# Kernel tuning notes

Measured on AMD Instinct MI355X. Metric: run time of the kernel, lower is better.

Reference implementation:

```python
import jax, jax.numpy as jnp
import numpy as np

QLEN, MLEN, BSZ = 1024, 1024, 2
D_MODEL, H, D_HEAD, D_FF = 1024, 16, 64, 4096
KLEN = QLEN + MLEN


def _ln(x, g, b, eps=1e-5):
    mu = jnp.mean(x, axis=-1, keepdims=True)
    var = jnp.var(x, axis=-1, keepdims=True)
    return (x - mu) * jax.lax.rsqrt(var + eps) * g + b


def _rel_shift(x):
    # x: [q, k, b, n] -> Transformer-XL relative shift
    q, k, b, n = x.shape
    zp = jnp.zeros((q, 1, b, n), x.dtype)
    xp = jnp.concatenate([zp, x], axis=1).reshape(k + 1, q, b, n)[1:]
    return xp.reshape(q, k, b, n)


def setup_inputs() -> dict:
    key = jax.random.key(0)
    ks = jax.random.split(key, 12)
    s = 0.02
    inp = {
        "input_": jax.random.normal(ks[0], (QLEN, BSZ, D_MODEL), jnp.float32),
        "mems": jax.random.normal(ks[1], (MLEN, BSZ, D_MODEL), jnp.float32),
        "pos_emb": jax.random.normal(ks[2], (KLEN, 1, D_MODEL), jnp.float32),
        # True = masked. Causal with memory: query i sees keys j <= i + MLEN
        "mask_tgt": jnp.triu(jnp.ones((QLEN, KLEN), bool), k=MLEN + 1),
        "ln1_g": jnp.ones((D_MODEL,), jnp.float32),
        "ln1_b": jnp.zeros((D_MODEL,), jnp.float32),
        "qkv_w": jax.random.normal(ks[3], (D_MODEL, 3 * H * D_HEAD), jnp.float32) * s,
        "qkv_b": jnp.zeros((3 * H * D_HEAD,), jnp.float32),
        "r_w": jax.random.normal(ks[4], (D_MODEL, H * D_HEAD), jnp.float32) * s,
        "r_w_bias": jax.random.normal(ks[5], (H, D_HEAD), jnp.float32) * s,
        "r_r_bias": jax.random.normal(ks[6], (H, D_HEAD), jnp.float32) * s,
        "o_w": jax.random.normal(ks[7], (H * D_HEAD, D_MODEL), jnp.float32) * s,
        "ln2_g": jnp.ones((D_MODEL,), jnp.float32),
        "ln2_b": jnp.zeros((D_MODEL,), jnp.float32),
        "ff_w1": jax.random.normal(ks[8], (D_MODEL, D_FF), jnp.float32) * s,
        "ff_b1": jnp.zeros((D_FF,), jnp.float32),
        "ff_w2": jax.random.normal(ks[9], (D_FF, D_MODEL), jnp.float32) * s,
        "ff_b2": jnp.zeros((D_MODEL,), jnp.float32),
    }
    return inp


def reference(input_, mems, pos_emb, mask_tgt, ln1_g, ln1_b, qkv_w, qkv_b,
              r_w, r_w_bias, r_r_bias, o_w, ln2_g, ln2_b,
              ff_w1, ff_b1, ff_w2, ff_b2):
    qlen, bsz, _ = input_.shape
    # --- pre-norm (applied to both current input and mems) ---
    q_in = _ln(input_, ln1_g, ln1_b)
    m_in = _ln(mems, ln1_g, ln1_b)
    cat = jnp.concatenate([m_in, q_in], axis=0)            # [klen, b, d]
    klen = cat.shape[0]
    heads = cat @ qkv_w + qkv_b                            # [klen, b, 3*h*dh]
    w_q, w_k, w_v = jnp.split(heads, 3, axis=-1)
    w_q = w_q[-qlen:].reshape(qlen, bsz, H, D_HEAD)        # [q, b, h, dh]
    w_k = w_k.reshape(klen, bsz, H, D_HEAD)
    w_v = w_v.reshape(klen, bsz, H, D_HEAD)
    r_k = (pos_emb[:, 0] @ r_w).reshape(klen, H, D_HEAD)   # [k, h, dh]

    AC = jnp.einsum('ibnd,jbnd->ijbn', w_q + r_w_bias, w_k)
    BD = jnp.einsum('ibnd,jnd->ijbn', w_q + r_r_bias, r_k)
    BD = _rel_shift(BD)
    scale = 1.0 / np.sqrt(D_HEAD)
    score = (AC + BD) * scale                              # [q, k, b, h]
    score = jnp.where(mask_tgt[:, :, None, None], -1e30, score)
    prob = jax.nn.softmax(score, axis=1)
    attn = jnp.einsum('ijbn,jbnd->ibnd', prob, w_v).reshape(qlen, bsz, H * D_HEAD)
    attn_out = attn @ o_w                                  # [q, b, d]
    x = input_ + attn_out                                  # residual (dropout = eval)

    # --- FFN block ---
    y = _ln(x, ln2_g, ln2_b)
    y = jax.nn.relu(y @ ff_w1 + ff_b1) @ ff_w2 + ff_b2
    return x + y
```

## Files before the change

### kernel.cpp

```cpp
#include <hip/hip_runtime.h>


typedef unsigned short u16;
typedef unsigned int   u32;
typedef __attribute__((ext_vector_type(8))) short bf16x8;
typedef __attribute__((ext_vector_type(4))) float f32x4;

struct alignas(16) U128 { u32 x[4]; };
struct alignas(16) F128 { float f[4]; };
struct alignas(8)  U64  { u32 x[2]; };

#define DEV static __device__ __forceinline__
#define MF(a, b, c) __builtin_amdgcn_mfma_f32_16x16x32_bf16((a), (b), (c), 0, 0, 0)

typedef __attribute__((address_space(1))) u32 as1_u32;
typedef __attribute__((address_space(3))) u32 as3_u32;
DEV void gload16(const void* g, void* l) {
  __builtin_amdgcn_global_load_lds((as1_u32*)g, (as3_u32*)l, 16, 0, 0);
}

DEV u16 f2bf(float f) {
  union { float f; u32 u; } v; v.f = f;
  u32 r = v.u + 0x7fffu + ((v.u >> 16) & 1u);
  return (u16)(r >> 16);
}
DEV float bf2f(u16 h) {
  union { u32 u; float f; } v; v.u = ((u32)h) << 16;
  return v.f;
}

__global__ __launch_bounds__(256) void ln_fuse(
    const u16* __restrict__ p0, const u16* __restrict__ p1,
    const u16* __restrict__ p2, const u16* __restrict__ p3,
    const float* __restrict__ resid, const float* __restrict__ g,
    const float* __restrict__ b, float* __restrict__ X, u16* __restrict__ YN)
{
  int row = blockIdx.x, tid = threadIdx.x;
  U64 a = ((const U64*)(p0 + (size_t)row * 1024))[tid];
  U64 c = ((const U64*)(p1 + (size_t)row * 1024))[tid];
  U64 d = ((const U64*)(p2 + (size_t)row * 1024))[tid];
  U64 e = ((const U64*)(p3 + (size_t)row * 1024))[tid];
  F128 rv = ((const F128*)(resid + (size_t)row * 1024))[tid];
  float x[4];
#pragma unroll
  for (int k = 0; k < 2; k++) {
    x[2*k]   = bf2f((u16)a.x[k]) + bf2f((u16)c.x[k]) + bf2f((u16)d.x[k]) + bf2f((u16)e.x[k]) + rv.f[2*k];
    x[2*k+1] = bf2f((u16)(a.x[k] >> 16)) + bf2f((u16)(c.x[k] >> 16)) + bf2f((u16)(d.x[k] >> 16)) + bf2f((u16)(e.x[k] >> 16)) + rv.f[2*k+1];
  }
  F128 xo;
#pragma unroll
  for (int j = 0; j < 4; j++) xo.f[j] = x[j];
  *(F128*)(X + (size_t)row * 1024 + tid * 4) = xo;

  float s = x[0] + x[1] + x[2] + x[3];
  float q = x[0]*x[0] + x[1]*x[1] + x[2]*x[2] + x[3]*x[3];
#pragma unroll
  for (int off = 1; off < 64; off <<= 1) {
    s += __shfl_xor(s, off); q += __shfl_xor(q, off);
  }
  __shared__ float sh[8];
  int wid = tid >> 6;
  if ((tid & 63) == 0) { sh[wid] = s; sh[4 + wid] = q; }
  __syncthreads();
  s = sh[0] + sh[1] + sh[2] + sh[3];
  q = sh[4] + sh[5] + sh[6] + sh[7];
  float mu = s * (1.0f / 1024.0f);
  float rs = rsqrtf(q * (1.0f / 1024.0f) - mu * mu + 1e-5f);
  F128 g4 = ((const F128*)g)[tid];
  F128 b4 = ((const F128*)b)[tid];
  union { u16 h[4]; U64 u; } o;
#pragma unroll
  for (int j = 0; j < 4; j++)
    o.h[j] = f2bf((x[j] - mu) * rs * g4.f[j] + b4.f[j]);
  *(U64*)(YN + (size_t)row * 1024 + tid * 4) = o.u;
}

__global__ __launch_bounds__(256) void prep_weights(
    const float* __restrict__ qkvw, const float* __restrict__ rw,
    const float* __restrict__ oww, const float* __restrict__ fw1,
    const float* __restrict__ fw2, const float* __restrict__ pos,
    const float* __restrict__ mems, const float* __restrict__ input_,
    const float* __restrict__ ln1g, const float* __restrict__ ln1b,
    u16* __restrict__ WT_QKV, u16* __restrict__ WT_R, u16* __restrict__ WT_O,
    u16* __restrict__ WT_F1, u16* __restrict__ WT_F2, u16* __restrict__ POSB,
    u16* __restrict__ CATLN)
{
  int id = blockIdx.x, tid = threadIdx.x;
  if (id >= 5376) {
    int row = id - 5376;
    const float* s_ = (row < 2048) ? mems + (size_t)row * 1024
                                   : input_ + (size_t)(row - 2048) * 1024;
    F128 v = ((const F128*)s_)[tid];
    float s = v.f[0] + v.f[1] + v.f[2] + v.f[3];
    float q = v.f[0]*v.f[0] + v.f[1]*v.f[1] + v.f[2]*v.f[2] + v.f[3]*v.f[3];
#pragma unroll
    for (int off = 1; off < 64; off <<= 1) {
      s += __shfl_xor(s, off); q += __shfl_xor(q, off);
    }
    __shared__ float sh[8];
    int wid = tid >> 6;
    if ((tid & 63) == 0) { sh[wid] = s; sh[4 + wid] = q; }
    __syncthreads();
    s = sh[0] + sh[1] + sh[2] + sh[3];
    q = sh[4] + sh[5] + sh[6] + sh[7];
    float mu = s * (1.0f / 1024.0f);
    float rs = rsqrtf(q * (1.0f / 1024.0f) - mu * mu + 1e-5f);
    F128 g4 = ((const F128*)ln1g)[tid];
    F128 b4 = ((const F128*)ln1b)[tid];
    union { u16 h[4]; U64 u; } o;
#pragma unroll
    for (int j = 0; j < 4; j++)
      o.h[j] = f2bf((v.f[j] - mu) * rs * g4.f[j] + b4.f[j]);
    *(U64*)(CATLN + (size_t)row * 1024 + tid * 4) = o.u;
    return;
  }
  if (id >= 3328) {
    int i = (id - 3328) * 256 + tid;
    F128 v = ((const F128*)pos)[i];
    union { u16 h[4]; U64 u; } o;
#pragma unroll
    for (int j = 0; j < 4; j++) o.h[j] = f2bf(v.f[j]);
    ((U64*)POSB)[i] = o.u;
    return;
  }
  const float* W; u16* Wt; int K, N, rem;
  if (id < 768)       { W = qkvw; Wt = WT_QKV; K = 1024; N = 3072; rem = id; }
  else if (id < 1024) { W = rw;   Wt = WT_R;   K = 1024; N = 1024; rem = id - 768; }
  else if (id < 1280) { W = oww;  Wt = WT_O;   K = 1024; N = 1024; rem = id - 1024; }
  else if (id < 2304) { W = fw1;  Wt = WT_F1;  K = 1024; N = 4096; rem = id - 1280; }
  else                { W = fw2;  Wt = WT_F2;  K = 4096; N = 1024; rem = id - 2304; }
  int nn = N >> 6;
  int k0 = (rem / nn) * 64, n0 = (rem % nn) * 64;
  __shared__ float t[64][65];
  int r = tid >> 6, c = tid & 63;
#pragma unroll
  for (int i = 0; i < 16; i++)
    t[r + i * 4][c] = W[(size_t)(k0 + r + i * 4) * N + n0 + c];
  __syncthreads();
#pragma unroll
  for (int i = 0; i < 16; i++) {
    int n = r + i * 4;
    Wt[(size_t)(n0 + n) * K + k0 + c] = f2bf(t[c][n]);
  }
}

template <int EPI, int NSPLIT>
__global__ __launch_bounds__(256, 2) void gemm_bt(
    const u16* __restrict__ A, const u16* __restrict__ Bt,
    u16* __restrict__ outb, const float* __restrict__ bias,
    u16* __restrict__ p0, u16* __restrict__ p1,
    u16* __restrict__ p2, u16* __restrict__ p3,
    int M, int N, int K)
{
  __shared__ u16 As[2][128 * 64];
  __shared__ u16 Bs[2][128 * 64];
  int tid = threadIdx.x;
  int m0 = blockIdx.x * 128, n0 = blockIdx.y * 128;
  int lane = tid & 63, wid = tid >> 6;
  int wr = wid >> 1, wc = wid & 1;
  f32x4 acc[4][4] = {};

  const int Kc = K / NSPLIT;
  const int kbase = (NSPLIT > 1) ? (int)blockIdx.z * Kc : 0;

  const int lrow = wid * 8 + (lane >> 3);
  const int lcol = 8 * ((lane & 7) ^ (lane >> 3));
  const u16* Ag = A  + (size_t)(m0 + lrow) * K + kbase + lcol;
  const u16* Bg = Bt + (size_t)(n0 + lrow) * K + kbase + lcol;

  auto stage = [&](int buf, int k0) {
#pragma unroll
    for (int i = 0; i < 4; i++) {
      gload16(Ag + (size_t)i * 32 * K + k0, &As[buf][(i * 4 + wid) * 512]);
      gload16(Bg + (size_t)i * 32 * K + k0, &Bs[buf][(i * 4 + wid) * 512]);
    }
  };

  const int rswz = 8 * (lane & 7);
  stage(0, 0);
  __syncthreads();
  int cur = 0;
  for (int k0 = 0; k0 < Kc; k0 += 64) {
    if (k0 + 64 < Kc) stage(cur ^ 1, k0 + 64);
    bf16x8 af[2][4], bfr[2][4];
#pragma unroll
    for (int kc = 0; kc < 2; kc++) {
      int cb = (kc * 32 + (lane >> 4) * 8) ^ rswz;
#pragma unroll
      for (int f = 0; f < 4; f++) {
        af[kc][f]  = *(const bf16x8*)&As[cur][(wr * 64 + f * 16 + (lane & 15)) * 64 + cb];
        bfr[kc][f] = *(const bf16x8*)&Bs[cur][(wc * 64 + f * 16 + (lane & 15)) * 64 + cb];
      }
    }
    __builtin_amdgcn_s_setprio(1);
#pragma unroll
    for (int kc = 0; kc < 2; kc++)
#pragma unroll
      for (int fi = 0; fi < 4; fi++)
#pragma unroll
        for (int fj = 0; fj < 4; fj++)
          acc[fi][fj] = MF(af[kc][fi], bfr[kc][fj], acc[fi][fj]);
    __builtin_amdgcn_s_setprio(0);
    __syncthreads();
    cur ^= 1;
  }

  u16* part = nullptr;
  if constexpr (NSPLIT > 1) {
    part = (blockIdx.z == 0) ? p0 : (blockIdx.z == 1) ? p1
         : (blockIdx.z == 2) ? p2 : p3;
  }
#pragma unroll
  for (int fi = 0; fi < 4; fi++)
#pragma unroll
    for (int fj = 0; fj < 4; fj++) {
      int col = n0 + wc * 64 + fj * 16 + (lane & 15);
      float bvv = (NSPLIT == 1 && bias != nullptr) ? bias[col] : 0.0f;
#pragma unroll
      for (int r = 0; r < 4; r++) {
        int row = m0 + wr * 64 + fi * 16 + (lane >> 4) * 4 + r;
        float v = acc[fi][fj][r] + bvv;
        if constexpr (NSPLIT > 1) {
          part[(size_t)row * N + col] = f2bf(v);
        } else {
          if constexpr (EPI == 1) v = fmaxf(v, 0.0f);
          outb[(size_t)row * N + col] = f2bf(v);
        }
      }
    }
}

template <int NS, int EPI>
__global__ __launch_bounds__(256) void reduce_splitb(
    const u16* __restrict__ p0, const u16* __restrict__ p1,
    const u16* __restrict__ p2, const u16* __restrict__ p3,
    const float* __restrict__ bias, const float* __restrict__ resid,
    u16* __restrict__ outb, float* __restrict__ outf, int N)
{
  int e = (blockIdx.x * 256 + threadIdx.x) * 8;
  U128 a = *(const U128*)(p0 + e);
  U128 c = *(const U128*)(p1 + e);
  float v[8];
#pragma unroll
  for (int k = 0; k < 4; k++) {
    v[2*k]   = bf2f((u16)a.x[k]) + bf2f((u16)c.x[k]);
    v[2*k+1] = bf2f((u16)(a.x[k] >> 16)) + bf2f((u16)(c.x[k] >> 16));
  }
  if constexpr (NS == 4) {
    U128 d2 = *(const U128*)(p2 + e);
    U128 d3 = *(const U128*)(p3 + e);
#pragma unroll
    for (int k = 0; k < 4; k++) {
      v[2*k]   += bf2f((u16)d2.x[k]) + bf2f((u16)d3.x[k]);
      v[2*k+1] += bf2f((u16)(d2.x[k] >> 16)) + bf2f((u16)(d3.x[k] >> 16));
    }
  }
  if constexpr (EPI == 2) {
    F128 r0 = *(const F128*)(resid + e);
    F128 r1 = *(const F128*)(resid + e + 4);
    int col = e % N;
    F128 o0, o1;
#pragma unroll
    for (int j = 0; j < 4; j++) {
      float b0 = (bias != nullptr) ? bias[col + j] : 0.0f;
      float b1 = (bias != nullptr) ? bias[col + 4 + j] : 0.0f;
      o0.f[j] = v[j] + b0 + r0.f[j];
      o1.f[j] = v[4 + j] + b1 + r1.f[j];
    }
    *(F128*)(outf + e) = o0;
    *(F128*)(outf + e + 4) = o1;
  } else {
    U128 o;
#pragma unroll
    for (int k = 0; k < 4; k++)
      o.x[k] = (u32)f2bf(v[2*k]) | ((u32)f2bf(v[2*k+1]) << 16);
    *(U128*)(outb + e) = o;
  }
}

__global__ __launch_bounds__(256) void extract_vt(
    const u16* __restrict__ heads, u16* __restrict__ Vt)
{
  __shared__ u16 t[64][72];
  int jt = blockIdx.x;
  int bh = blockIdx.y;
  int b = bh >> 4, h = bh & 15;
  int tid = threadIdx.x;
  int row = tid >> 2;
  int cc = (tid & 3) * 16;
#pragma unroll
  for (int i = 0; i < 2; i++)
    *(U128*)&t[row][cc + i * 8] =
        *(const U128*)&heads[(size_t)((jt * 64 + row) * 2 + b) * 3072 + 2048 + h * 64 + cc + i * 8];
  __syncthreads();
  int jc = tid & 63, dr = tid >> 6;
#pragma unroll
  for (int i = 0; i < 16; i++) {
    int d = dr + i * 4;
    Vt[((size_t)bh * 64 + d) * 2048 + jt * 64 + jc] = t[jc][d];
  }
}

__global__ __launch_bounds__(256, 2) void attn_fwd(
    const u16* __restrict__ heads, const u16* __restrict__ rk,
    const u16* __restrict__ Vt, const float* __restrict__ rwb,
    const float* __restrict__ rrb, u16* __restrict__ attnout)
{
  __shared__ u16 lds[37376];

  int tid = threadIdx.x, lane = tid & 63, wid = tid >> 6;
  int bh = blockIdx.x;
  int y = (int)blockIdx.y;
  int xt = (y < 8) ? y : 23 - y;
  int i0 = xt * 64;
  int b = bh >> 4, h = bh & 15;
  const float SCL = 0.18033688f;

  u16* Ps = lds + 32768;
  u16* Qw = lds;
  u16* Qr = lds + 4608;

  for (int c = tid; c < 512; c += 256) {
    int row = c >> 3, c8 = (c & 7) * 8;
    union { U128 v; u16 h[8]; } in, ow, orr;
    in.v = *(const U128*)&heads[(size_t)((1024 + i0 + row) * 2 + b) * 3072 + h * 64 + c8];
#pragma unroll
    for (int j = 0; j < 8; j++) {
      float q = bf2f(in.h[j]);
      ow.h[j]  = f2bf(q + rwb[h * 64 + c8 + j]);
      orr.h[j] = f2bf(q + rrb[h * 64 + c8 + j]);
    }
    *(U128*)&Qw[row * 72 + c8] = ow.v;
    *(U128*)&Qr[row * 72 + c8] = orr.v;
  }
  __syncthreads();

  bf16x8 qwf[2], qrf[2];
  int qrow = wid * 16 + (lane & 15);
#pragma unroll
  for (int kc = 0; kc < 2; kc++) {
    qwf[kc] = *(const bf16x8*)&Qw[qrow * 72 + kc * 32 + (lane >> 4) * 8];
    qrf[kc] = *(const bf16x8*)&Qr[qrow * 72 + kc * 32 + (lane >> 4) * 8];
  }
  __syncthreads();

  const int srow = lane >> 3;
  const int scol = 8 * ((lane & 7) ^ srow);

  auto stage = [&](int buf, int t) {
    int j0 = t * 64;
    u16* base = lds + buf * 16384;
#pragma unroll
    for (int i = 0; i < 2; i++) {
      int g8 = wid * 2 + i;
      int jr = j0 + g8 * 8 + srow;
      gload16(heads + (size_t)(jr * 2 + b) * 3072 + 1024 + h * 64 + scol,
              base + g8 * 512);
    }
#pragma unroll
    for (int i = 0; i < 2; i++) {
      int g8 = wid * 2 + i;
      int dr = g8 * 8 + srow;
      gload16(Vt + ((size_t)bh * 64 + dr) * 2048 + j0 + scol,
              base + 4096 + g8 * 512);
    }
    int rbase = 960 + j0 - i0;
#pragma unroll
    for (int i = 0; i < 4; i++) {
      int g8 = wid * 4 + i;
      int rr = rbase + g8 * 8 + srow;
      rr = rr < 0 ? 0 : (rr > 2047 ? 2047 : rr);
      gload16(rk + (size_t)rr * 1024 + h * 64 + scol,
              base + 8192 + g8 * 512);
    }
  };

  stage(0, 0);
  __syncthreads();

  float mrow[4], plrow[4];
  f32x4 o[4] = {};
  f32x4 bd[5];
#pragma unroll
  for (int r = 0; r < 4; r++) { mrow[r] = -1e30f; plrow[r] = 0.0f; }

  int nt = i0 / 64 + 17;
  const int roffw = 48 - wid * 16;
  const int g = lane >> 4, cc = lane & 15;
  const int rswz = 8 * (lane & 7);

  for (int t = 0; t < nt; t++) {
    const u16* base = lds + (t & 1) * 16384;
    if (t + 1 < nt) stage((t + 1) & 1, t + 1);

    const u16* Kb = base;
    const u16* Vb = base + 4096;
    const u16* Rb = base + 8192;

    f32x4 sAC[4] = {};
    if (t == 0) bd[0] = (f32x4){0.f, 0.f, 0.f, 0.f};
#pragma unroll
    for (int fb = 1; fb < 5; fb++) bd[fb] = (f32x4){0.f, 0.f, 0.f, 0.f};
    __builtin_amdgcn_s_setprio(1);
#pragma unroll
    for (int kc = 0; kc < 2; kc++) {
      int cb = (kc * 32 + g * 8) ^ rswz;
#pragma unroll
      for (int fj = 0; fj < 4; fj++) {
        bf16x8 kf = *(const bf16x8*)&Kb[(fj * 16 + (lane & 15)) * 64 + cb];
        sAC[fj] = MF(qwf[kc], kf, sAC[fj]);
      }
      if (t == 0) {
        bf16x8 rf = *(const bf16x8*)&Rb[(roffw + (lane & 15)) * 64 + cb];
        bd[0] = MF(qrf[kc], rf, bd[0]);
      }
#pragma unroll
      for (int fb = 1; fb < 5; fb++) {
        bf16x8 rf = *(const bf16x8*)&Rb[(roffw + fb * 16 + (lane & 15)) * 64 + cb];
        bd[fb] = MF(qrf[kc], rf, bd[fb]);
      }
    }
    __builtin_amdgcn_s_setprio(0);

    float p[4][4];
#pragma unroll
    for (int fj = 0; fj < 4; fj++)
#pragma unroll
      for (int r = 0; r < 4; r++) {
        int sh_ = 15 - 4 * g - r;
        int src = (lane & 48) | ((lane + sh_) & 15);
        float lo = __shfl(bd[fj][r], src);
        float hi = __shfl(bd[fj + 1][r], src);
        float bdv = (cc + sh_ < 16) ? lo : hi;
        p[fj][r] = (sAC[fj][r] + bdv) * SCL;
      }
    bd[0] = bd[4];

    if (t == nt - 1) {
#pragma unroll
      for (int fj = 0; fj < 4; fj++)
#pragma unroll
        for (int r = 0; r < 4; r++)
          if (fj * 16 + cc > 16 * wid + 4 * g + r) p[fj][r] = -1e30f;
    }

    float tmax[4];
#pragma unroll
    for (int r = 0; r < 4; r++)
      tmax[r] = fmaxf(fmaxf(p[0][r], p[1][r]), fmaxf(p[2][r], p[3][r]));

    bool ok = true;
#pragma unroll
    for (int r = 0; r < 4; r++) ok &= (tmax[r] <= mrow[r] + 12.0f);
    if (!__all(ok)) {
#pragma unroll
      for (int off = 1; off < 16; off <<= 1)
#pragma unroll
        for (int r = 0; r < 4; r++)
          tmax[r] = fmaxf(tmax[r], __shfl_xor(tmax[r], off));
#pragma unroll
      for (int r = 0; r < 4; r++) {
        float mn = fmaxf(mrow[r], tmax[r]);
        float ms = exp2f(mrow[r] - mn);
        mrow[r] = mn;
        plrow[r] *= ms;
#pragma unroll
        for (int fd = 0; fd < 4; fd++) o[fd][r] *= ms;
      }
    }

#pragma unroll
    for (int fj = 0; fj < 4; fj++)
#pragma unroll
      for (int r = 0; r < 4; r++) {
        float e = exp2f(p[fj][r] - mrow[r]);
        plrow[r] += e;
        Ps[(wid * 16 + (lane >> 4) * 4 + r) * 72 + fj * 16 + (lane & 15)] = f2bf(e);
      }
    __builtin_amdgcn_s_setprio(1);
#pragma unroll
    for (int kc = 0; kc < 2; kc++) {
      bf16x8 pf = *(const bf16x8*)&Ps[(wid * 16 + (lane & 15)) * 72 + kc * 32 + g * 8];
      int cb = (kc * 32 + g * 8) ^ rswz;
#pragma unroll
      for (int fd = 0; fd < 4; fd++) {
        bf16x8 vf = *(const bf16x8*)&Vb[(fd * 16 + (lane & 15)) * 64 + cb];
        o[fd] = MF(pf, vf, o[fd]);
      }
    }
    __builtin_amdgcn_s_setprio(0);

    __syncthreads();
  }

#pragma unroll
  for (int off = 1; off < 16; off <<= 1)
#pragma unroll
    for (int r = 0; r < 4; r++)
      plrow[r] += __shfl_xor(plrow[r], off);
#pragma unroll
  for (int fd = 0; fd < 4; fd++)
#pragma unroll
    for (int r = 0; r < 4; r++) {
      int ii2 = (lane >> 4) * 4 + r;
      int row = (i0 + wid * 16 + ii2) * 2 + b;
      attnout[(size_t)row * 1024 + h * 64 + fd * 16 + (lane & 15)] = f2bf(o[fd][r] / plrow[r]);
    }
}

extern "C" void kernel_launch(void* const* d_in, const int* in_sizes, int n_in,
                              void* d_out, int out_size, void* d_ws, size_t ws_size,
                              hipStream_t stream)
{
  const float* input_ = (const float*)d_in[0];
  const float* mems   = (const float*)d_in[1];
  const float* pos    = (const float*)d_in[2];
  const float* ln1g = (const float*)d_in[4];
  const float* ln1b = (const float*)d_in[5];
  const float* qkvw = (const float*)d_in[6];
  const float* qkvb = (const float*)d_in[7];
  const float* rw   = (const float*)d_in[8];
  const float* rwb  = (const float*)d_in[9];
  const float* rrb  = (const float*)d_in[10];
  const float* ow   = (const float*)d_in[11];
  const float* ln2g = (const float*)d_in[12];
  const float* ln2b = (const float*)d_in[13];
  const float* fw1  = (const float*)d_in[14];
  const float* fb1  = (const float*)d_in[15];
  const float* fw2  = (const float*)d_in[16];
  const float* fb2  = (const float*)d_in[17];
  float* out = (float*)d_out;

  char* w = (char*)d_ws;
  u16* WT_QKV = (u16*)(w + 0);
  u16* WT_R   = (u16*)(w + 6291456);
  u16* WT_O   = (u16*)(w + 8388608);
  u16* WT_F1  = (u16*)(w + 10485760);
  u16* WT_F2  = (u16*)(w + 18874368);
  u16* POSB   = (u16*)(w + 27262976);
  u16* ATTN   = POSB;
  u16* CATLN  = (u16*)(w + 31457280);
  u16* HEADS  = (u16*)(w + 39845888);
  u16* H1     = HEADS;
  float* X    = (float*)(w + 56623104);
  u16* RK     = (u16*)(w + 65011712);
  u16* VT     = (u16*)(w + 69206016);
  u16* YN     = VT;

  u16* RKP0 = (u16*)(w + 31457280);
  u16* RKP1 = (u16*)(w + 35651584);
  u16* RKP2 = (u16*)(w + 69206016);
  u16* RKP3 = (u16*)(w + 73400320);
  u16* OWP0 = (u16*)(w + 39845888);
  u16* OWP1 = (u16*)(w + 44040192);
  u16* OWP2 = (u16*)(w + 48234496);
  u16* OWP3 = (u16*)(w + 52428800);
  u16* F2P0 = (u16*)(w + 0);
  u16* F2P1 = (u16*)(w + 10485760);
  u16* F2P2 = (u16*)(w + 31457280);
  u16* F2P3 = (u16*)(w + 65011712);

  dim3 blk(256);

  prep_weights<<<dim3(9472), blk, 0, stream>>>(
      qkvw, rw, ow, fw1, fw2, pos, mems, input_, ln1g, ln1b,
      WT_QKV, WT_R, WT_O, WT_F1, WT_F2, POSB, CATLN);

  gemm_bt<0, 1><<<dim3(32, 24), blk, 0, stream>>>(
      CATLN, WT_QKV, HEADS, qkvb, nullptr, nullptr, nullptr, nullptr, 4096, 3072, 1024);
  gemm_bt<0, 4><<<dim3(16, 8, 4), blk, 0, stream>>>(
      POSB, WT_R, nullptr, nullptr, RKP0, RKP1, RKP2, RKP3, 2048, 1024, 1024);
  reduce_splitb<4, 0><<<dim3(1024), blk, 0, stream>>>(
      RKP0, RKP1, RKP2, RKP3, nullptr, nullptr, RK, nullptr, 1024);

  extract_vt<<<dim3(32, 32), blk, 0, stream>>>(HEADS, VT);
  attn_fwd<<<dim3(32, 16), blk, 0, stream>>>(HEADS, RK, VT, rwb, rrb, ATTN);

  gemm_bt<0, 4><<<dim3(16, 8, 4), blk, 0, stream>>>(
      ATTN, WT_O, nullptr, nullptr, OWP0, OWP1, OWP2, OWP3, 2048, 1024, 1024);
  ln_fuse<<<dim3(2048), blk, 0, stream>>>(
      OWP0, OWP1, OWP2, OWP3, input_, ln2g, ln2b, X, YN);

  gemm_bt<1, 1><<<dim3(16, 32), blk, 0, stream>>>(
      YN, WT_F1, H1, fb1, nullptr, nullptr, nullptr, nullptr, 2048, 4096, 1024);
  gemm_bt<0, 4><<<dim3(16, 8, 4), blk, 0, stream>>>(
      H1, WT_F2, nullptr, nullptr, F2P0, F2P1, F2P2, F2P3, 2048, 1024, 4096);
  reduce_splitb<4, 2><<<dim3(1024), blk, 0, stream>>>(
      F2P0, F2P1, F2P2, F2P3, fb2, X, nullptr, out, 1024);
}
```

Before: 215.8 us.

## Skip memory-row Q projection and fuse r_k GEMM into QKV launch

Remaps the QKV GEMM grid so Q columns are computed only for the query rows, since memory-row queries are discarded. The positional r_k projection is folded into the same launch as extra tiles, replacing the separate split-K GEMM and its reduction kernel. This removes redundant FLOPs, two launches, and partial-sum traffic. The r_k tiles now run without split-K, so fewer blocks share that part of the work.

After: 208.9 us. 3.2% less time.

```diff
diff --git a/kernel.cpp b/kernel.cpp
--- a/kernel.cpp
+++ b/kernel.cpp
@@ -144,10 +144,10 @@
   }
 }
 
-template <int EPI, int NSPLIT>
+template <int EPI, int NSPLIT, int MAP = 0>
 __global__ __launch_bounds__(256, 2) void gemm_bt(
-    const u16* __restrict__ A, const u16* __restrict__ Bt,
-    u16* __restrict__ outb, const float* __restrict__ bias,
+    const u16* __restrict__ A_, const u16* __restrict__ Bt_,
+    u16* __restrict__ outb_, const float* __restrict__ bias_,
     u16* __restrict__ p0, u16* __restrict__ p1,
     u16* __restrict__ p2, u16* __restrict__ p3,
     int M, int N, int K)
@@ -155,7 +155,21 @@
   __shared__ u16 As[2][128 * 64];
   __shared__ u16 Bs[2][128 * 64];
   int tid = threadIdx.x;
-  int m0 = blockIdx.x * 128, n0 = blockIdx.y * 128;
+  const u16* A = A_; const u16* Bt = Bt_;
+  u16* outb = outb_; const float* bias = bias_;
+  int m0, n0, Nst = N;
+  if constexpr (MAP == 2) {
+    int id = blockIdx.x;
+    if (id < 512) { m0 = (id >> 4) * 128; n0 = 1024 + (id & 15) * 128; }
+    else if (id < 640) { int i2 = id - 512; m0 = 2048 + (i2 >> 3) * 128; n0 = (i2 & 7) * 128; }
+    else {
+      int i2 = id - 640;
+      m0 = (i2 >> 3) * 128; n0 = (i2 & 7) * 128;
+      A = p0; Bt = p1; outb = p2; bias = nullptr; Nst = 1024;
+    }
+  } else {
+    m0 = blockIdx.x * 128; n0 = blockIdx.y * 128;
+  }
   int lane = tid & 63, wid = tid >> 6;
   int wr = wid >> 1, wc = wid & 1;
   f32x4 acc[4][4] = {};
@@ -221,10 +235,10 @@
         int row = m0 + wr * 64 + fi * 16 + (lane >> 4) * 4 + r;
         float v = acc[fi][fj][r] + bvv;
         if constexpr (NSPLIT > 1) {
-          part[(size_t)row * N + col] = f2bf(v);
+          part[(size_t)row * Nst + col] = f2bf(v);
         } else {
           if constexpr (EPI == 1) v = fmaxf(v, 0.0f);
-          outb[(size_t)row * N + col] = f2bf(v);
+          outb[(size_t)row * Nst + col] = f2bf(v);
         }
       }
     }
@@ -547,10 +561,6 @@
   u16* VT     = (u16*)(w + 69206016);
   u16* YN     = VT;
 
-  u16* RKP0 = (u16*)(w + 31457280);
-  u16* RKP1 = (u16*)(w + 35651584);
-  u16* RKP2 = (u16*)(w + 69206016);
-  u16* RKP3 = (u16*)(w + 73400320);
   u16* OWP0 = (u16*)(w + 39845888);
   u16* OWP1 = (u16*)(w + 44040192);
   u16* OWP2 = (u16*)(w + 48234496);
@@ -566,12 +576,8 @@
       qkvw, rw, ow, fw1, fw2, pos, mems, input_, ln1g, ln1b,
       WT_QKV, WT_R, WT_O, WT_F1, WT_F2, POSB, CATLN);
 
-  gemm_bt<0, 1><<<dim3(32, 24), blk, 0, stream>>>(
-      CATLN, WT_QKV, HEADS, qkvb, nullptr, nullptr, nullptr, nullptr, 4096, 3072, 1024);
-  gemm_bt<0, 4><<<dim3(16, 8, 4), blk, 0, stream>>>(
-      POSB, WT_R, nullptr, nullptr, RKP0, RKP1, RKP2, RKP3, 2048, 1024, 1024);
-  reduce_splitb<4, 0><<<dim3(1024), blk, 0, stream>>>(
-      RKP0, RKP1, RKP2, RKP3, nullptr, nullptr, RK, nullptr, 1024);
+  gemm_bt<0, 1, 2><<<dim3(768), blk, 0, stream>>>(
+      CATLN, WT_QKV, HEADS, qkvb, POSB, WT_R, RK, nullptr, 4096, 3072, 1024);
 
   extract_vt<<<dim3(32, 32), blk, 0, stream>>>(HEADS, VT);
   attn_fwd<<<dim3(32, 16), blk, 0, stream>>>(HEADS, RK, VT, rwb, rrb, ATTN);
```
